# Optimization experiments

Hardware: AMD Instinct MI355X
Metric: run time of the kernel (lower is better)

The kernel has to match this reference:

```python
import jax, jax.numpy as jnp
import numpy as np

DIM, SEQ, HEADS, HDIM, BATCH, VOCAB, NVOCAB = 512, 1024, 8, 64, 8, 1024, 3
EPS = 1e-5


def layer_norm(x, g, b):
    mu = x.mean(-1, keepdims=True)
    var = x.var(-1, keepdims=True)
    return (x - mu) * jax.lax.rsqrt(var + EPS) * g + b


def multiscale_retention(x, Wq, Wk, Wv, Wg, Wo):
    B, S, D = x.shape
    def split(h):  # [B,S,D] -> [B,H,S,hd]
        return h.reshape(B, S, HEADS, HDIM).transpose(0, 2, 1, 3)
    q, k, v = split(x @ Wq), split(x @ Wk), split(x @ Wv)
    # RetNet per-head decays and causal decay matrix D[h,n,m] = gamma_h^(n-m), n>=m
    gammas = 1.0 - 2.0 ** (-5.0 - jnp.arange(HEADS, dtype=jnp.float32))
    n = jnp.arange(S)
    diff = n[:, None] - n[None, :]
    decay = jnp.where(diff >= 0, gammas[:, None, None] ** jnp.maximum(diff, 0).astype(jnp.float32), 0.0)
    scores = jnp.einsum('bhsd,bhtd->bhst', q, k) * (1.0 / np.sqrt(HDIM))
    y = jnp.einsum('bhst,bhtd->bhsd', scores * decay, v)
    # group norm per head (no affine)
    mu = y.mean(-1, keepdims=True)
    var = y.var(-1, keepdims=True)
    y = (y - mu) * jax.lax.rsqrt(var + EPS)
    y = y.transpose(0, 2, 1, 3).reshape(B, S, D)
    gate = jax.nn.swish(x @ Wg)
    return (gate * y) @ Wo


def feed_forward(x, W1, b1, W2, b2):
    return jax.nn.relu(x @ W1 + b1) @ W2 + b2


def setup_inputs() -> dict:
    key = jax.random.key(0)
    ks = jax.random.split(key, 12)
    s = 0.02
    return {
        'ids': jax.random.randint(ks[0], (NVOCAB, BATCH, SEQ), 0, VOCAB),
        'emb_tables': jax.random.normal(ks[1], (NVOCAB, VOCAB, DIM), jnp.float32) * s,
        'pos_emb': jax.random.normal(ks[2], (NVOCAB, SEQ, DIM), jnp.float32) * s,
        'ln_gamma': jnp.ones((DIM,), jnp.float32),
        'ln_beta': jnp.zeros((DIM,), jnp.float32),
        'Wq': jax.random.normal(ks[3], (DIM, DIM), jnp.float32) * s,
        'Wk': jax.random.normal(ks[4], (DIM, DIM), jnp.float32) * s,
        'Wv': jax.random.normal(ks[5], (DIM, DIM), jnp.float32) * s,
        'Wg': jax.random.normal(ks[6], (DIM, DIM), jnp.float32) * s,
        'Wo': jax.random.normal(ks[7], (DIM, DIM), jnp.float32) * s,
        'W1': jax.random.normal(ks[8], (DIM, DIM), jnp.float32) * s,
        'b1': jnp.zeros((DIM,), jnp.float32),
        'W2': jax.random.normal(ks[9], (DIM, DIM), jnp.float32) * s,
        'b2': jnp.zeros((DIM,), jnp.float32),
        'fc_W': jax.random.normal(ks[10], (SEQ * DIM, 1), jnp.float32) * s,
        'fc_b': jnp.zeros((1,), jnp.float32),
    }


def reference(ids, emb_tables, pos_emb, ln_gamma, ln_beta, Wq, Wk, Wv, Wg, Wo,
              W1, b1, W2, b2, fc_W, fc_b):
    x = None
    for i in range(NVOCAB):  # loop over vocab embeddings, x overwritten each pass (as in source)
        emb = emb_tables[i][ids[i]] + pos_emb[i][None, :, :]  # [B,S,D]
        x = layer_norm(emb, ln_gamma, ln_beta)
        x = multiscale_retention(x, Wq, Wk, Wv, Wg, Wo) + x
        x = feed_forward(layer_norm(x, ln_gamma, ln_beta), W1, b1, W2, b2) + x
        x = layer_norm(x, ln_gamma, ln_beta)
    flat = x.reshape(x.shape[0], -1)  # Flatten
    return jax.nn.sigmoid(flat @ fc_W + fc_b)  # dropout inactive at inference
```

## Files before the change

kernel.cpp:

```cpp
#include <hip/hip_runtime.h>
#include <math.h>

typedef unsigned short u16;
typedef __attribute__((ext_vector_type(8))) _Float16 half8;
typedef __attribute__((ext_vector_type(4))) float f32x4;
typedef __attribute__((ext_vector_type(4))) unsigned short us4;


static __device__ __forceinline__ u16 f2h(float f) {
    _Float16 h = (_Float16)f;
    return __builtin_bit_cast(u16, h);
}
static __device__ __forceinline__ float h2f(u16 u) {
    return (float)__builtin_bit_cast(_Float16, u);
}
static __device__ __forceinline__ void gl_lds16(const void* g, void* l) {
    __builtin_amdgcn_global_load_lds(
        (const __attribute__((address_space(1))) void*)g,
        (__attribute__((address_space(3))) void*)l, 16, 0, 0);
}

__global__ __launch_bounds__(256) void prep_kernel(
    const float* __restrict__ Wq, const float* __restrict__ Wk, const float* __restrict__ Wv,
    const float* __restrict__ Wg, const float* __restrict__ Wo, const float* __restrict__ W1,
    const float* __restrict__ W2, u16* __restrict__ WT,
    const int* __restrict__ ids, const float* __restrict__ emb, const float* __restrict__ pos,
    const float* __restrict__ gam, const float* __restrict__ bet, u16* __restrict__ x0h)
{
    __shared__ float tile[64][65];
    int bx = blockIdx.x, t = threadIdx.x;
    if (bx < 448) {
        const float* Ws[7] = {Wq, Wk, Wv, Wg, Wo, W1, W2};
        int w = bx >> 6, rem = bx & 63;
        int k0 = (rem >> 3) * 64, n0 = (rem & 7) * 64;
        const float* W = Ws[w];
        for (int c = t; c < 4096; c += 256) {
            int row = c >> 6, col = c & 63;
            tile[row][col] = W[(size_t)(k0 + row) * 512 + n0 + col];
        }
        __syncthreads();
        for (int c = t; c < 4096; c += 256) {
            int row = c >> 6, col = c & 63;
            WT[(size_t)w * 262144 + (size_t)(n0 + row) * 512 + k0 + col] = f2h(tile[col][row]);
        }
    } else {
        int wid = t >> 6, lane = t & 63;
        int row = (bx - 448) * 4 + wid;
        int col = lane * 8;
        int id = ids[2 * 8192 + row];
        const float* e = emb + (size_t)(2 * 1024 + id) * 512 + col;
        const float* p = pos + (size_t)(2 * 1024 + (row & 1023)) * 512 + col;
        float4 e0 = *(const float4*)e, e1 = *(const float4*)(e + 4);
        float4 p0 = *(const float4*)p, p1 = *(const float4*)(p + 4);
        float v[8] = {e0.x + p0.x, e0.y + p0.y, e0.z + p0.z, e0.w + p0.w,
                      e1.x + p1.x, e1.y + p1.y, e1.z + p1.z, e1.w + p1.w};
        float s1 = 0.f, s2 = 0.f;
#pragma unroll
        for (int j = 0; j < 8; ++j) { s1 += v[j]; s2 += v[j] * v[j]; }
#pragma unroll
        for (int o = 32; o >= 1; o >>= 1) {
            s1 += __shfl_xor(s1, o, 64);
            s2 += __shfl_xor(s2, o, 64);
        }
        float mu = s1 * (1.f / 512.f);
        float var = fmaxf(s2 * (1.f / 512.f) - mu * mu, 0.f);
        float rs = 1.f / sqrtf(var + 1e-5f);
        float4 g0 = *(const float4*)&gam[col], g1 = *(const float4*)&gam[col + 4];
        float4 b0 = *(const float4*)&bet[col], b1 = *(const float4*)&bet[col + 4];
        float gv[8] = {g0.x, g0.y, g0.z, g0.w, g1.x, g1.y, g1.z, g1.w};
        float bv[8] = {b0.x, b0.y, b0.z, b0.w, b1.x, b1.y, b1.z, b1.w};
        half8 hv;
#pragma unroll
        for (int j = 0; j < 8; ++j) hv[j] = (_Float16)((v[j] - mu) * rs * gv[j] + bv[j]);
        *(half8*)&x0h[(size_t)row * 512 + col] = hv;
    }
}

__global__ __launch_bounds__(256) void ln_kernel(
    const u16* __restrict__ xin,
    const float* __restrict__ gam, const float* __restrict__ bet,
    u16* __restrict__ outh,
    const float* __restrict__ fcW, float* __restrict__ fcpart)
{
    int wid = threadIdx.x >> 6, lane = threadIdx.x & 63;
    int row = blockIdx.x * 4 + wid;
    int col = lane * 8;
    float v[8];
    half8 x = *(const half8*)&xin[(size_t)row * 512 + col];
#pragma unroll
    for (int j = 0; j < 8; ++j) v[j] = (float)x[j];
    float s1 = 0.f, s2 = 0.f;
#pragma unroll
    for (int j = 0; j < 8; ++j) { s1 += v[j]; s2 += v[j] * v[j]; }
#pragma unroll
    for (int o = 32; o >= 1; o >>= 1) {
        s1 += __shfl_xor(s1, o, 64);
        s2 += __shfl_xor(s2, o, 64);
    }
    float mu = s1 * (1.f / 512.f);
    float var = fmaxf(s2 * (1.f / 512.f) - mu * mu, 0.f);
    float rs = 1.f / sqrtf(var + 1e-5f);
    float4 g0 = *(const float4*)&gam[col], g1 = *(const float4*)&gam[col + 4];
    float4 b0 = *(const float4*)&bet[col], b1 = *(const float4*)&bet[col + 4];
    float gv[8] = {g0.x, g0.y, g0.z, g0.w, g1.x, g1.y, g1.z, g1.w};
    float bv[8] = {b0.x, b0.y, b0.z, b0.w, b1.x, b1.y, b1.z, b1.w};
    float y[8];
#pragma unroll
    for (int j = 0; j < 8; ++j) y[j] = (v[j] - mu) * rs * gv[j] + bv[j];
    if (outh) {
        half8 hv;
#pragma unroll
        for (int j = 0; j < 8; ++j) hv[j] = (_Float16)y[j];
        *(half8*)&outh[(size_t)row * 512 + col] = hv;
    }
    if (fcW) {
        int srow = row & 1023;
        const float* wp = &fcW[(size_t)srow * 512 + col];
        float4 w0 = *(const float4*)wp, w1 = *(const float4*)(wp + 4);
        float d = y[0] * w0.x + y[1] * w0.y + y[2] * w0.z + y[3] * w0.w +
                  y[4] * w1.x + y[5] * w1.y + y[6] * w1.z + y[7] * w1.w;
#pragma unroll
        for (int o = 32; o >= 1; o >>= 1) d += __shfl_xor(d, o, 64);
        if (lane == 0) fcpart[row] = d;
    }
}

static __device__ __forceinline__ void stage_tile(
    const u16* pa0, const u16* pa1, const u16* pb0, const u16* pb1,
    u16* ldsw, int slot, int kt)
{
    int off = kt * 32;
    u16* d = ldsw + slot * 16384;
    gl_lds16(pa0 + off, d);
    gl_lds16(pa1 + off, d + 4096);
    gl_lds16(pb0 + off, d + 8192);
    gl_lds16(pb1 + off, d + 12288);
}

static __device__ __forceinline__ void compute_tile(
    const u16* lds, int slot, int wm, int wn, int quad, int l15, f32x4 (&acc)[8][4])
{
    const u16* A = lds + slot * 16384;
    const u16* B = A + 8192;
    __builtin_amdgcn_s_setprio(1);
#pragma unroll
    for (int mq = 0; mq < 2; ++mq)
#pragma unroll
        for (int nq = 0; nq < 2; ++nq) {
            half8 a[4], b[2];
#pragma unroll
            for (int i = 0; i < 4; ++i)
                a[i] = *(const half8*)&A[(wm * 128 + mq * 64 + i * 16 + l15) * 32 + quad * 8];
#pragma unroll
            for (int j = 0; j < 2; ++j)
                b[j] = *(const half8*)&B[(wn * 64 + nq * 32 + j * 16 + l15) * 32 + quad * 8];
#pragma unroll
            for (int i = 0; i < 4; ++i)
#pragma unroll
                for (int j = 0; j < 2; ++j)
                    acc[mq * 4 + i][nq * 2 + j] = __builtin_amdgcn_mfma_f32_16x16x32_f16(
                        a[i], b[j], acc[mq * 4 + i][nq * 2 + j], 0, 0, 0);
        }
    __builtin_amdgcn_s_setprio(0);
}

#define QITER(KT, VM)                                                              \
    do {                                                                           \
        if ((KT) + 3 < 16) stage_tile(pa0, pa1, pb0, pb1, ldsw, ((KT) + 3) & 3, (KT) + 3); \
        asm volatile("s_waitcnt vmcnt(" #VM ")" ::: "memory");                     \
        __builtin_amdgcn_s_barrier();                                              \
        asm volatile("" ::: "memory");                                             \
        compute_tile(lds, (KT) & 3, wm, wn, quad, l15, acc);                       \
        asm volatile("" ::: "memory");                                             \
        __builtin_amdgcn_s_barrier();                                              \
    } while (0)

__global__ __launch_bounds__(512, 2) void gemm_f16(
    const u16* __restrict__ A2, const u16* __restrict__ Bg,
    u16* __restrict__ outh, int ostride)
{
    __shared__ u16 lds[65536];
    int t = threadIdx.x;
    int wid = t >> 6, lane = t & 63, quad = lane >> 4, l15 = lane & 15;
    int wm = wid >> 2, wn = wid & 3;
    int orig = blockIdx.x;
    int wgid = (orig & 7) * 32 + (orig >> 3);
    int m0 = (wgid >> 3) * 256, n0 = (wgid & 7) * 256;

    int srow = t >> 2, sc = (t & 3) * 8;
    const u16* pa0 = A2 + (size_t)(m0 + srow) * 512 + sc;
    const u16* pa1 = pa0 + (size_t)128 * 512;
    const u16* pb0 = Bg + (size_t)(n0 + srow) * 512 + sc;
    const u16* pb1 = pb0 + (size_t)128 * 512;
    u16* ldsw = lds + wid * 512;

    f32x4 acc[8][4];
#pragma unroll
    for (int i = 0; i < 8; ++i)
#pragma unroll
        for (int j = 0; j < 4; ++j) acc[i][j] = (f32x4){0.f, 0.f, 0.f, 0.f};

    stage_tile(pa0, pa1, pb0, pb1, ldsw, 0, 0);
    stage_tile(pa0, pa1, pb0, pb1, ldsw, 1, 1);
    stage_tile(pa0, pa1, pb0, pb1, ldsw, 2, 2);

    QITER(0, 12);  QITER(1, 12);  QITER(2, 12);  QITER(3, 12);
    QITER(4, 12);  QITER(5, 12);  QITER(6, 12);  QITER(7, 12);
    QITER(8, 12);  QITER(9, 12);  QITER(10, 12); QITER(11, 12);
    QITER(12, 12);
    QITER(13, 8);  QITER(14, 4);  QITER(15, 0);

    u16* C = lds;
#pragma unroll
    for (int i = 0; i < 8; ++i)
#pragma unroll
        for (int j = 0; j < 4; ++j)
#pragma unroll
            for (int r = 0; r < 4; ++r)
                C[(wm * 128 + i * 16 + quad * 4 + r) * 256 + wn * 64 + j * 16 + l15] =
                    f2h(acc[i][j][r]);
    __builtin_amdgcn_s_barrier();
    asm volatile("" ::: "memory");
#pragma unroll
    for (int it = 0; it < 16; ++it) {
        int idx = it * 512 + t;
        int row = idx >> 5, ch = idx & 31;
        *(half8*)&outh[(size_t)(m0 + row) * ostride + n0 + ch * 8] =
            *(const half8*)&C[row * 256 + ch * 8];
    }
}

__global__ __launch_bounds__(256) void gemm_f16_n64(
    const u16* __restrict__ A2, const u16* __restrict__ Bg,
    u16* __restrict__ outh,
    const u16* __restrict__ res, const float* __restrict__ bias, int mode)
{
    __shared__ u16 As[128 * 64];
    __shared__ u16 Bs[64 * 64];
    int t = threadIdx.x;
    int wid = t >> 6, lane = t & 63, quad = lane >> 4, l15 = lane & 15;
    int orig = blockIdx.x;
    int wgid = (orig & 7) * 64 + (orig >> 3);
    int m0 = (wgid >> 3) * 128, n0 = (wgid & 7) * 64;

    int srow = wid * 8 + (lane >> 3);
    int scol = (lane & 7) * 8;

    f32x4 acc[2][4];
#pragma unroll
    for (int a = 0; a < 2; ++a)
#pragma unroll
        for (int b = 0; b < 4; ++b) acc[a][b] = (f32x4){0.f, 0.f, 0.f, 0.f};

    for (int ki = 0; ki < 8; ++ki) {
        int k0 = ki * 64;
        __syncthreads();
#pragma unroll
        for (int i = 0; i < 4; ++i) {
            int r = i * 32 + srow;
            gl_lds16(&A2[(size_t)(m0 + r) * 512 + k0 + scol], &As[(i * 32 + wid * 8) * 64]);
        }
#pragma unroll
        for (int i = 0; i < 2; ++i) {
            int r = i * 32 + srow;
            gl_lds16(&Bg[(size_t)(n0 + r) * 512 + k0 + scol], &Bs[(i * 32 + wid * 8) * 64]);
        }
        __syncthreads();
#pragma unroll
        for (int ks = 0; ks < 2; ++ks) {
            half8 af[2], bf[4];
#pragma unroll
            for (int tm = 0; tm < 2; ++tm)
                af[tm] = *(const half8*)&As[(wid * 32 + tm * 16 + l15) * 64 + ks * 32 + quad * 8];
#pragma unroll
            for (int tn = 0; tn < 4; ++tn)
                bf[tn] = *(const half8*)&Bs[(tn * 16 + l15) * 64 + ks * 32 + quad * 8];
#pragma unroll
            for (int tm = 0; tm < 2; ++tm)
#pragma unroll
                for (int tn = 0; tn < 4; ++tn)
                    acc[tm][tn] = __builtin_amdgcn_mfma_f32_16x16x32_f16(af[tm], bf[tn], acc[tm][tn], 0, 0, 0);
        }
    }

    __syncthreads();
#pragma unroll
    for (int tm = 0; tm < 2; ++tm) {
#pragma unroll
        for (int tn = 0; tn < 4; ++tn) {
            int n = n0 + tn * 16 + l15;
#pragma unroll
            for (int r = 0; r < 4; ++r) {
                int rl = wid * 32 + tm * 16 + quad * 4 + r;
                int m = m0 + rl;
                float v = acc[tm][tn][r];
                if (mode == 1) v += h2f(res[(size_t)m * 512 + n]);
                else if (mode == 2) v = fmaxf(v + bias[n], 0.f);
                else if (mode == 3) v += bias[n] + h2f(res[(size_t)m * 512 + n]);
                As[rl * 64 + tn * 16 + l15] = f2h(v);
            }
        }
    }
    __syncthreads();
#pragma unroll
    for (int i = 0; i < 4; ++i) {
        int c = t + i * 256;
        int row = c >> 3, ch = c & 7;
        *(half8*)&outh[(size_t)(m0 + row) * 512 + n0 + ch * 8] =
            *(const half8*)&As[row * 64 + ch * 8];
    }
}

__global__ __launch_bounds__(256) void chunk_t(
    const u16* __restrict__ QKVGh, u16* __restrict__ Tst)
{
    __shared__ u16 kth[64 * 144];
    __shared__ u16 vth[64 * 144];
    int t = threadIdx.x;
    int wid = t >> 6, lane = t & 63, quad = lane >> 4, l15 = lane & 15;
    int bh = blockIdx.x >> 3, c = blockIdx.x & 7;
    int b = bh >> 3, h = bh & 7;
    float gamma = 1.f - exp2f(-(float)(5 + h));
    float l2g = log2f(gamma);

    for (int cc = t; cc < 2048; cc += 256) {
        int d = cc & 63, mseg = cc >> 6;
        size_t gbase = (size_t)(b * 1024 + c * 128 + mseg * 4) * 2048 + h * 64 + d;
        us4 k4, v4;
#pragma unroll
        for (int i = 0; i < 4; ++i) {
            float kv = h2f(QKVGh[gbase + 512 + (size_t)i * 2048]);
            k4[i] = f2h(kv * exp2f((float)(127 - (mseg * 4 + i)) * l2g));
            v4[i] = QKVGh[gbase + 1024 + (size_t)i * 2048];
        }
        int base = d * 144 + (((mseg >> 1) + d) & 15) * 8 + (mseg & 1) * 4;
        *(us4*)&kth[base] = k4;
        *(us4*)&vth[base] = v4;
    }
    __syncthreads();
    f32x4 T[4];
#pragma unroll
    for (int dt = 0; dt < 4; ++dt) T[dt] = (f32x4){0.f, 0.f, 0.f, 0.f};
    int ra = wid * 16 + l15;
#pragma unroll
    for (int ks = 0; ks < 4; ++ks) {
        half8 av = *(const half8*)&vth[ra * 144 + ((ks * 4 + quad + ra) & 15) * 8];
#pragma unroll
        for (int dt = 0; dt < 4; ++dt) {
            int rb = dt * 16 + l15;
            half8 bk = *(const half8*)&kth[rb * 144 + ((ks * 4 + quad + rb) & 15) * 8];
            T[dt] = __builtin_amdgcn_mfma_f32_16x16x32_f16(av, bk, T[dt], 0, 0, 0);
        }
    }
#pragma unroll
    for (int dt = 0; dt < 4; ++dt)
#pragma unroll
        for (int r = 0; r < 4; ++r) {
            int i = wid * 16 + quad * 4 + r;
            int j = dt * 16 + l15;
            Tst[(((size_t)bh * 8 + c) * 64 + i) * 64 + j] = f2h(T[dt][r]);
        }
}

__global__ __launch_bounds__(256) void retention_f16(
    const u16* __restrict__ QKVGh, const u16* __restrict__ Tst, u16* __restrict__ Zh)
{
    __shared__ u16 kh[128 * 64];
    __shared__ u16 vth[64 * 144];
    __shared__ u16 ph[4][16 * 132];

    int t = threadIdx.x;
    int wid = t >> 6, lane = t & 63, quad = lane >> 4, l15 = lane & 15;
    int bh = blockIdx.x >> 3, qt = blockIdx.x & 7;
    int b = bh >> 3, h = bh & 7;
    int n0 = qt * 128;

    float gamma = 1.f - exp2f(-(float)(5 + h));
    float l2g = log2f(gamma);

    {
        int srow = wid * 8 + (lane >> 3);
        int scol = (lane & 7) * 8;
#pragma unroll
        for (int i = 0; i < 4; ++i) {
            int r = i * 32 + srow;
            gl_lds16(&QKVGh[(size_t)(b * 1024 + n0 + r) * 2048 + 512 + h * 64 + scol],
                     &kh[(i * 32 + wid * 8) * 64]);
        }
    }
    for (int c = t; c < 2048; c += 256) {
        int d = c & 63, mseg = c >> 6;
        size_t gbase = (size_t)(b * 1024 + n0 + mseg * 4) * 2048 + 1024 + h * 64 + d;
        us4 v4 = {QKVGh[gbase], QKVGh[gbase + 2048],
                  QKVGh[gbase + 4096], QKVGh[gbase + 6144]};
        int base = d * 144 + (((mseg >> 1) + d) & 15) * 8 + (mseg & 1) * 4;
        *(us4*)&vth[base] = v4;
    }

    half8 aH[2][2], aHs[2][2];
#pragma unroll
    for (int g = 0; g < 2; ++g) {
        int rowloc = wid * 32 + g * 16 + l15;
        int qrow = b * 1024 + n0 + rowloc;
        const u16* qp = QKVGh + (size_t)qrow * 2048 + h * 64;
        float qs = exp2f((float)(rowloc + 1) * l2g - 3.f);
#pragma unroll
        for (int ks = 0; ks < 2; ++ks) {
            aH[g][ks] = *(const half8*)&qp[ks * 32 + quad * 8];
#pragma unroll
            for (int j = 0; j < 8; ++j)
                aHs[g][ks][j] = (_Float16)((float)aH[g][ks][j] * qs);
        }
    }

    half8 sf[2][4];
    if (qt > 0) {
        float sa[2][4][8];
#pragma unroll
        for (int ks = 0; ks < 2; ++ks)
#pragma unroll
            for (int dt = 0; dt < 4; ++dt)
#pragma unroll
                for (int j = 0; j < 8; ++j) sa[ks][dt][j] = 0.f;
        for (int c = 0; c < qt; ++c) {
            float sc = exp2f((float)(128 * (qt - 1 - c)) * l2g);
            const u16* tp = &Tst[((size_t)bh * 8 + c) * 4096];
#pragma unroll
            for (int ks = 0; ks < 2; ++ks)
#pragma unroll
                for (int dt = 0; dt < 4; ++dt) {
                    half8 tv = *(const half8*)&tp[(dt * 16 + l15) * 64 + ks * 32 + quad * 8];
#pragma unroll
                    for (int j = 0; j < 8; ++j) sa[ks][dt][j] += sc * (float)tv[j];
                }
        }
#pragma unroll
        for (int ks = 0; ks < 2; ++ks)
#pragma unroll
            for (int dt = 0; dt < 4; ++dt)
#pragma unroll
                for (int j = 0; j < 8; ++j) sf[ks][dt][j] = (_Float16)sa[ks][dt][j];
    }
    __syncthreads();

    f32x4 yacc[2][4];
#pragma unroll
    for (int g = 0; g < 2; ++g)
#pragma unroll
        for (int dt = 0; dt < 4; ++dt) yacc[g][dt] = (f32x4){0.f, 0.f, 0.f, 0.f};

    if (qt > 0) {
#pragma unroll
        for (int ks = 0; ks < 2; ++ks)
#pragma unroll
            for (int g = 0; g < 2; ++g)
#pragma unroll
                for (int dt = 0; dt < 4; ++dt)
                    yacc[g][dt] = __builtin_amdgcn_mfma_f32_16x16x32_f16(aHs[g][ks], sf[ks][dt], yacc[g][dt], 0, 0, 0);
    }

#pragma unroll
    for (int g = 0; g < 2; ++g) {
        f32x4 sacc[8];
#pragma unroll
        for (int tn = 0; tn < 8; ++tn) sacc[tn] = (f32x4){0.f, 0.f, 0.f, 0.f};
#pragma unroll
        for (int tn = 0; tn < 8; ++tn)
#pragma unroll
            for (int ks = 0; ks < 2; ++ks) {
                half8 bH = *(const half8*)&kh[(tn * 16 + l15) * 64 + ks * 32 + quad * 8];
                sacc[tn] = __builtin_amdgcn_mfma_f32_16x16x32_f16(aH[g][ks], bH, sacc[tn], 0, 0, 0);
            }
#pragma unroll
        for (int tn = 0; tn < 8; ++tn) {
            int mloc = tn * 16 + l15;
#pragma unroll
            for (int r = 0; r < 4; ++r) {
                int nloc = wid * 32 + g * 16 + quad * 4 + r;
                int diff = nloc - mloc;
                float p = (diff >= 0) ? sacc[tn][r] * exp2f((float)diff * l2g - 3.0f) : 0.f;
                ph[wid][(quad * 4 + r) * 132 + tn * 16 + l15] = f2h(p);
            }
        }
        half8 pH[4];
#pragma unroll
        for (int ks = 0; ks < 4; ++ks)
            pH[ks] = *(const half8*)&ph[wid][l15 * 132 + ks * 32 + quad * 8];
#pragma unroll
        for (int dt = 0; dt < 4; ++dt) {
            int d = dt * 16 + l15;
#pragma unroll
            for (int ks = 0; ks < 4; ++ks) {
                half8 vv = *(const half8*)&vth[d * 144 + ((ks * 4 + quad + d) & 15) * 8];
                yacc[g][dt] = __builtin_amdgcn_mfma_f32_16x16x32_f16(pH[ks], vv, yacc[g][dt], 0, 0, 0);
            }
        }
    }

#pragma unroll
    for (int g = 0; g < 2; ++g) {
#pragma unroll
        for (int r = 0; r < 4; ++r) {
            float s1 = yacc[g][0][r] + yacc[g][1][r] + yacc[g][2][r] + yacc[g][3][r];
            float s2 = yacc[g][0][r] * yacc[g][0][r] + yacc[g][1][r] * yacc[g][1][r] +
                       yacc[g][2][r] * yacc[g][2][r] + yacc[g][3][r] * yacc[g][3][r];
#pragma unroll
            for (int o = 1; o <= 8; o <<= 1) {
                s1 += __shfl_xor(s1, o, 64);
                s2 += __shfl_xor(s2, o, 64);
            }
            float mu = s1 * (1.f / 64.f);
            float var = fmaxf(s2 * (1.f / 64.f) - mu * mu, 0.f);
            float rs = 1.f / sqrtf(var + 1e-5f);
            int nglob = n0 + wid * 32 + g * 16 + quad * 4 + r;
            size_t grow = (size_t)(b * 1024 + nglob);
#pragma unroll
            for (int dt = 0; dt < 4; ++dt) {
                int d = dt * 16 + l15;
                float yv = (yacc[g][dt][r] - mu) * rs;
                float gt = h2f(QKVGh[grow * 2048 + 1536 + h * 64 + d]);
                float sw = gt / (1.f + expf(-gt));
                Zh[grow * 512 + h * 64 + d] = f2h(yv * sw);
            }
        }
    }
}

__global__ __launch_bounds__(256) void fc_final(const float* __restrict__ fcpart,
                                                const float* __restrict__ fcb,
                                                float* __restrict__ out)
{
    __shared__ float red[4];
    int b = blockIdx.x, t = threadIdx.x;
    float4 v = *(const float4*)&fcpart[(size_t)b * 1024 + t * 4];
    float s = v.x + v.y + v.z + v.w;
    int wid = t >> 6, lane = t & 63;
#pragma unroll
    for (int o = 32; o >= 1; o >>= 1) s += __shfl_xor(s, o, 64);
    if (lane == 0) red[wid] = s;
    __syncthreads();
    if (t == 0) {
        float l = red[0] + red[1] + red[2] + red[3] + fcb[0];
        out[b] = 1.f / (1.f + expf(-l));
    }
}

extern "C" void kernel_launch(void* const* d_in, const int* in_sizes, int n_in,
                              void* d_out, int out_size, void* d_ws, size_t ws_size,
                              hipStream_t stream)
{
    const int* ids = (const int*)d_in[0];
    const float* emb = (const float*)d_in[1];
    const float* pos = (const float*)d_in[2];
    const float* ln_g = (const float*)d_in[3];
    const float* ln_b = (const float*)d_in[4];
    const float* Wq = (const float*)d_in[5];
    const float* Wk = (const float*)d_in[6];
    const float* Wv = (const float*)d_in[7];
    const float* Wg = (const float*)d_in[8];
    const float* Wo = (const float*)d_in[9];
    const float* W1 = (const float*)d_in[10];
    const float* b1 = (const float*)d_in[11];
    const float* W2 = (const float*)d_in[12];
    const float* b2 = (const float*)d_in[13];
    const float* fcW = (const float*)d_in[14];
    const float* fcb = (const float*)d_in[15];
    float* out = (float*)d_out;

    char* ws = (char*)d_ws;
    u16* WT     = (u16*)(ws);
    u16* x0h    = (u16*)(ws + 3670016);
    u16* Zh     = (u16*)(ws + 12058624);
    u16* QKVGh  = (u16*)(ws + 20447232);
    float* fcpart = (float*)(ws + 54001664);
    u16* Tst    = (u16*)(ws + 54034432);
    u16* X1h = QKVGh;
    u16* Th  = (u16*)((char*)QKVGh + 8388608);
    u16* Hh  = (u16*)((char*)QKVGh + 16777216);
    u16* X2h = Zh;

    prep_kernel<<<2496, 256, 0, stream>>>(Wq, Wk, Wv, Wg, Wo, W1, W2, WT,
                                          ids, emb, pos, ln_g, ln_b, x0h);
    gemm_f16<<<256, 512, 0, stream>>>(x0h, WT, QKVGh, 2048);
    chunk_t<<<512, 256, 0, stream>>>(QKVGh, Tst);
    retention_f16<<<512, 256, 0, stream>>>(QKVGh, Tst, Zh);
    gemm_f16_n64<<<512, 256, 0, stream>>>(Zh, WT + 4 * 262144, X1h, x0h, nullptr, 1);
    ln_kernel<<<2048, 256, 0, stream>>>(X1h, ln_g, ln_b, Th, nullptr, nullptr);
    gemm_f16_n64<<<512, 256, 0, stream>>>(Th, WT + 5 * 262144, Hh, nullptr, b1, 2);
    gemm_f16_n64<<<512, 256, 0, stream>>>(Hh, WT + 6 * 262144, X2h, X1h, b2, 3);
    ln_kernel<<<2048, 256, 0, stream>>>(X2h, ln_g, ln_b, nullptr, fcW, fcpart);
    fc_final<<<8, 256, 0, stream>>>(fcpart, fcb, out);
}
```

Before: 213.2 us.

## Rewrite N=512 GEMM with 128x128 tiles and 4-stage async LDS pipeline

Replaces the 128x64-tile, 256-thread single-buffered GEMM used for Wo/W1/W2 with a 128x128-tile, 512-thread kernel that runs a 4-slot ring of global_load_lds stages over K in 32-wide steps, fully unrolled, with explicit vmcnt waits and s_setprio around the MFMA blocks. It aims to overlap global loads with MFMA work and to cut redundant A reloads by halving the number of tiles. The trade-off is only 256 blocks, which on a many-CU chip may underfill the device, plus 64KB of LDS per block, which limits occupancy.

```diff
diff --git a/kernel.cpp b/kernel.cpp
--- a/kernel.cpp
+++ b/kernel.cpp
@@ -230,84 +230,106 @@
     }
 }
 
-__global__ __launch_bounds__(256) void gemm_f16_n64(
+static __device__ __forceinline__ void stage_n64(
+    const u16* pa, const u16* pb, u16* ldsw, int slot, int kt)
+{
+    int off = kt * 32;
+    u16* d = ldsw + slot * 8192;
+    gl_lds16(pa + off, d);
+    gl_lds16(pb + off, d + 4096);
+}
+
+static __device__ __forceinline__ void compute_n64(
+    const u16* lds, int slot, int wm, int wn, int quad, int l15, f32x4 (&acc)[4][2])
+{
+    const u16* A = lds + slot * 8192;
+    const u16* B = A + 4096;
+    __builtin_amdgcn_s_setprio(1);
+    half8 a[4], b[2];
+#pragma unroll
+    for (int i = 0; i < 4; ++i)
+        a[i] = *(const half8*)&A[(wm * 64 + i * 16 + l15) * 32 + quad * 8];
+#pragma unroll
+    for (int j = 0; j < 2; ++j)
+        b[j] = *(const half8*)&B[(wn * 32 + j * 16 + l15) * 32 + quad * 8];
+#pragma unroll
+    for (int i = 0; i < 4; ++i)
+#pragma unroll
+        for (int j = 0; j < 2; ++j)
+            acc[i][j] = __builtin_amdgcn_mfma_f32_16x16x32_f16(a[i], b[j], acc[i][j], 0, 0, 0);
+    __builtin_amdgcn_s_setprio(0);
+}
+
+#define NITER(KT, VM)                                                          \
+    do {                                                                       \
+        if ((KT) + 3 < 16) stage_n64(pa, pb, ldsw, ((KT) + 3) & 3, (KT) + 3);  \
+        asm volatile("s_waitcnt vmcnt(" #VM ")" ::: "memory");                 \
+        __builtin_amdgcn_s_barrier();                                          \
+        asm volatile("" ::: "memory");                                         \
+        compute_n64(lds, (KT) & 3, wm, wn, quad, l15, acc);                    \
+        asm volatile("" ::: "memory");                                         \
+        __builtin_amdgcn_s_barrier();                                          \
+    } while (0)
+
+__global__ __launch_bounds__(512, 2) void gemm_f16_n64(
     const u16* __restrict__ A2, const u16* __restrict__ Bg,
     u16* __restrict__ outh,
     const u16* __restrict__ res, const float* __restrict__ bias, int mode)
 {
-    __shared__ u16 As[128 * 64];
-    __shared__ u16 Bs[64 * 64];
+    __shared__ u16 lds[32768];
     int t = threadIdx.x;
     int wid = t >> 6, lane = t & 63, quad = lane >> 4, l15 = lane & 15;
+    int wm = wid >> 2, wn = wid & 3;
     int orig = blockIdx.x;
-    int wgid = (orig & 7) * 64 + (orig >> 3);
-    int m0 = (wgid >> 3) * 128, n0 = (wgid & 7) * 64;
-
-    int srow = wid * 8 + (lane >> 3);
-    int scol = (lane & 7) * 8;
-
-    f32x4 acc[2][4];
-#pragma unroll
-    for (int a = 0; a < 2; ++a)
-#pragma unroll
-        for (int b = 0; b < 4; ++b) acc[a][b] = (f32x4){0.f, 0.f, 0.f, 0.f};
-
-    for (int ki = 0; ki < 8; ++ki) {
-        int k0 = ki * 64;
-        __syncthreads();
-#pragma unroll
-        for (int i = 0; i < 4; ++i) {
-            int r = i * 32 + srow;
-            gl_lds16(&A2[(size_t)(m0 + r) * 512 + k0 + scol], &As[(i * 32 + wid * 8) * 64]);
-        }
-#pragma unroll
-        for (int i = 0; i < 2; ++i) {
-            int r = i * 32 + srow;
-            gl_lds16(&Bg[(size_t)(n0 + r) * 512 + k0 + scol], &Bs[(i * 32 + wid * 8) * 64]);
-        }
-        __syncthreads();
-#pragma unroll
-        for (int ks = 0; ks < 2; ++ks) {
-            half8 af[2], bf[4];
-#pragma unroll
-            for (int tm = 0; tm < 2; ++tm)
-                af[tm] = *(const half8*)&As[(wid * 32 + tm * 16 + l15) * 64 + ks * 32 + quad * 8];
-#pragma unroll
-            for (int tn = 0; tn < 4; ++tn)
-                bf[tn] = *(const half8*)&Bs[(tn * 16 + l15) * 64 + ks * 32 + quad * 8];
-#pragma unroll
-            for (int tm = 0; tm < 2; ++tm)
-#pragma unroll
-                for (int tn = 0; tn < 4; ++tn)
-                    acc[tm][tn] = __builtin_amdgcn_mfma_f32_16x16x32_f16(af[tm], bf[tn], acc[tm][tn], 0, 0, 0);
-        }
-    }
-
-    __syncthreads();
-#pragma unroll
-    for (int tm = 0; tm < 2; ++tm) {
-#pragma unroll
-        for (int tn = 0; tn < 4; ++tn) {
-            int n = n0 + tn * 16 + l15;
+    int wgid = (orig & 7) * 32 + (orig >> 3);
+    int m0 = (wgid >> 2) * 128, n0 = (wgid & 3) * 128;
+
+    int srow = t >> 2, sc = (t & 3) * 8;
+    const u16* pa = A2 + (size_t)(m0 + srow) * 512 + sc;
+    const u16* pb = Bg + (size_t)(n0 + srow) * 512 + sc;
+    u16* ldsw = lds + wid * 512;
+
+    f32x4 acc[4][2];
+#pragma unroll
+    for (int i = 0; i < 4; ++i)
+#pragma unroll
+        for (int j = 0; j < 2; ++j) acc[i][j] = (f32x4){0.f, 0.f, 0.f, 0.f};
+
+    stage_n64(pa, pb, ldsw, 0, 0);
+    stage_n64(pa, pb, ldsw, 1, 1);
+    stage_n64(pa, pb, ldsw, 2, 2);
+
+    NITER(0, 6);  NITER(1, 6);  NITER(2, 6);  NITER(3, 6);
+    NITER(4, 6);  NITER(5, 6);  NITER(6, 6);  NITER(7, 6);
+    NITER(8, 6);  NITER(9, 6);  NITER(10, 6); NITER(11, 6);
+    NITER(12, 6);
+    NITER(13, 4); NITER(14, 2); NITER(15, 0);
+
+#pragma unroll
+    for (int i = 0; i < 4; ++i)
+#pragma unroll
+        for (int j = 0; j < 2; ++j) {
+            int nl = wn * 32 + j * 16 + l15;
+            int n = n0 + nl;
 #pragma unroll
             for (int r = 0; r < 4; ++r) {
-                int rl = wid * 32 + tm * 16 + quad * 4 + r;
+                int rl = wm * 64 + i * 16 + quad * 4 + r;
                 int m = m0 + rl;
-                float v = acc[tm][tn][r];
+                float v = acc[i][j][r];
                 if (mode == 1) v += h2f(res[(size_t)m * 512 + n]);
                 else if (mode == 2) v = fmaxf(v + bias[n], 0.f);
                 else if (mode == 3) v += bias[n] + h2f(res[(size_t)m * 512 + n]);
-                As[rl * 64 + tn * 16 + l15] = f2h(v);
+                lds[rl * 128 + nl] = f2h(v);
             }
         }
-    }
-    __syncthreads();
-#pragma unroll
-    for (int i = 0; i < 4; ++i) {
-        int c = t + i * 256;
-        int row = c >> 3, ch = c & 7;
+    __builtin_amdgcn_s_barrier();
+    asm volatile("" ::: "memory");
+#pragma unroll
+    for (int it = 0; it < 4; ++it) {
+        int idx = it * 512 + t;
+        int row = idx >> 4, ch = idx & 15;
         *(half8*)&outh[(size_t)(m0 + row) * 512 + n0 + ch * 8] =
-            *(const half8*)&As[row * 64 + ch * 8];
+            *(const half8*)&lds[row * 128 + ch * 8];
     }
 }
 
@@ -584,10 +606,10 @@
     gemm_f16<<<256, 512, 0, stream>>>(x0h, WT, QKVGh, 2048);
     chunk_t<<<512, 256, 0, stream>>>(QKVGh, Tst);
     retention_f16<<<512, 256, 0, stream>>>(QKVGh, Tst, Zh);
-    gemm_f16_n64<<<512, 256, 0, stream>>>(Zh, WT + 4 * 262144, X1h, x0h, nullptr, 1);
+    gemm_f16_n64<<<256, 512, 0, stream>>>(Zh, WT + 4 * 262144, X1h, x0h, nullptr, 1);
     ln_kernel<<<2048, 256, 0, stream>>>(X1h, ln_g, ln_b, Th, nullptr, nullptr);
-    gemm_f16_n64<<<512, 256, 0, stream>>>(Th, WT + 5 * 262144, Hh, nullptr, b1, 2);
-    gemm_f16_n64<<<512, 256, 0, stream>>>(Hh, WT + 6 * 262144, X2h, X1h, b2, 3);
+    gemm_f16_n64<<<256, 512, 0, stream>>>(Th, WT + 5 * 262144, Hh, nullptr, b1, 2);
+    gemm_f16_n64<<<256, 512, 0, stream>>>(Hh, WT + 6 * 262144, X2h, X1h, b2, 3);
     ln_kernel<<<2048, 256, 0, stream>>>(X2h, ln_g, ln_b, nullptr, fcW, fcpart);
     fc_final<<<8, 256, 0, stream>>>(fcpart, fcb, out);
 }
```

Measured after the change: 210.2 us. Within noise of the previous version (-1.4%).
